# Performance work log

Hardware: AMD Instinct MI355X
Metric: run time of the kernel (lower is better)

The kernel has to match this reference:

```python
import jax, jax.numpy as jnp
import numpy as np


def setup_inputs() -> dict:
    key = jax.random.key(0)
    k1, k2, k3 = jax.random.split(key, 3)
    I, H, W, C, N = 8, 240, 320, 128, 100000
    img_feats = jax.random.normal(k1, (I, H, W, C), dtype=jnp.float32)
    pcd_feats = jax.random.normal(k2, (N, C), dtype=jnp.float32)
    # pixel coords in [0, 360): values >= H (or >= W) are masked out, mimicking
    # points that project outside the image (compute_masks)
    pcd_pixels = jax.random.randint(k3, (I, N, 2), 0, 360, dtype=jnp.int32)
    return {"img_feats": img_feats, "pcd_feats": pcd_feats, "pcd_pixels": pcd_pixels}


def reference(img_feats, pcd_feats, pcd_pixels):
    # img_feats: [I, H, W, C], pcd_feats: [N, C], pcd_pixels: [I, N, 2] (h, w)
    I, H, W, C = img_feats.shape
    N = pcd_feats.shape[0]
    h = pcd_pixels[..., 0]
    w = pcd_pixels[..., 1]
    # compute_masks: in-bounds check
    mask = (h >= 0) & (h < H) & (w >= 0) & (w < W)            # [I, N] bool
    m = mask.astype(img_feats.dtype)                          # [I, N]
    hc = jnp.clip(h, 0, H - 1)
    wc = jnp.clip(w, 0, W - 1)
    flat_hw = hc * W + wc                                     # [I, N]

    # ---- collect_img_feats: gather image feats at pixels, mean over images per point
    gathered = jnp.take_along_axis(
        img_feats.reshape(I, H * W, C), flat_hw[..., None], axis=1
    )                                                         # [I, N, C]
    pcd_counts = m.sum(axis=0)                                # [N]
    pcd_from_img = (gathered * m[..., None]).sum(axis=0) / jnp.clip(
        pcd_counts, 1e-10
    )[:, None]                                                # [N, C]

    # ---- collect_pcd_feats: scatter point feats into image grid, mean per pixel
    flat_idx = (jnp.arange(I, dtype=flat_hw.dtype)[:, None] * (H * W) + flat_hw).reshape(-1)  # [I*N]
    src = (pcd_feats[None, :, :] * m[..., None]).reshape(-1, C)                               # [I*N, C]
    img_sum = jnp.zeros((I * H * W, C), img_feats.dtype).at[flat_idx].add(src)
    img_cnt = jnp.zeros((I * H * W,), img_feats.dtype).at[flat_idx].add(m.reshape(-1))
    img_from_pcd = (img_sum / jnp.clip(img_cnt, 1e-10)[:, None]).reshape(I, H, W, C)

    return pcd_from_img, img_from_pcd
```

## Files before the change

### kernel.cpp

```cpp
#include <hip/hip_runtime.h>

#define IMGS 8
#define HH 240
#define WW 320
#define CC 128
#define HW (HH * WW)
#define ELEMS (IMGS * HW)

#define CAP 16

typedef float f4 __attribute__((ext_vector_type(4)));

__global__ __launch_bounds__(256) void zero_counts_kernel(uint4* __restrict__ p)
{
    int t = blockIdx.x * 256 + threadIdx.x;
    if (t < ELEMS / 4) p[t] = make_uint4(0u, 0u, 0u, 0u);
}

__global__ __launch_bounds__(256) void count_fill_kernel(
    const int* __restrict__ pix,
    unsigned*  __restrict__ counts,
    unsigned*  __restrict__ list,
    int N)
{
    int n = blockIdx.x * 256 + threadIdx.x;
    int i = blockIdx.y;
    if (n >= N) return;
    int2 hw = *reinterpret_cast<const int2*>(pix + ((size_t)i * N + n) * 2);
    int h = hw.x, w = hw.y;
    if (h >= 0 && h < HH && w >= 0 && w < WW) {
        int p = i * HW + h * WW + w;
        unsigned slot = atomicAdd(&counts[p], 1u);
        if (slot < CAP) list[(size_t)p * CAP + slot] = (unsigned)n;
    }
}

#define GB 12500
#define TOTAL 89600

__global__ __launch_bounds__(256) void mega_kernel(
    const float*    __restrict__ img,
    const int*      __restrict__ pix,
    const float*    __restrict__ pcd,
    const unsigned* __restrict__ counts,
    const unsigned* __restrict__ list,
    float*          __restrict__ out_pcd,
    float*          __restrict__ out_img,
    int N)
{
    int bid = blockIdx.x;
    if (bid % 7 == 0) {
        int gb = bid / 7;
        if (gb >= GB) return;
        int tid   = gb * 256 + threadIdx.x;
        int point = tid >> 5;
        int lane  = tid & 31;

        int2 hw[IMGS];
#pragma unroll
        for (int i = 0; i < IMGS; ++i)
            hw[i] = *reinterpret_cast<const int2*>(pix + ((size_t)i * N + point) * 2);

        f4    v[IMGS];
        float m[IMGS];
#pragma unroll
        for (int i = 0; i < IMGS; ++i) {
            int h = hw[i].x, w = hw[i].y;
            bool ok = (h >= 0) & (h < HH) & (w >= 0) & (w < WW);
            int hc = min(max(h, 0), HH - 1);
            int wc = min(max(w, 0), WW - 1);
            v[i] = reinterpret_cast<const f4*>(
                       img + ((size_t)i * HW + (size_t)hc * WW + wc) * CC)[lane];
            m[i] = ok ? 1.f : 0.f;
        }

        f4 acc = {0.f, 0.f, 0.f, 0.f};
        float cnt = 0.f;
#pragma unroll
        for (int i = 0; i < IMGS; ++i) {
            acc += v[i] * m[i];
            cnt += m[i];
        }
        float inv = 1.f / fmaxf(cnt, 1e-10f);
        acc *= inv;
        __builtin_nontemporal_store(
            acc, reinterpret_cast<f4*>(out_pcd + (size_t)point * CC) + lane);
    } else {
        int ob   = bid - bid / 7 - 1;
        int tid  = ob * 256 + threadIdx.x;
        int p    = tid >> 5;
        int lane = tid & 31;

        unsigned kc = counts[p];
        unsigned k  = kc < CAP ? kc : CAP;
        const uint4* lp4 = reinterpret_cast<const uint4*>(list + (size_t)p * CAP);

        f4 acc = {0.f, 0.f, 0.f, 0.f};
        for (unsigned base = 0; base < k; base += 4) {
            uint4 L = lp4[base >> 2];
            unsigned id[4] = {L.x, L.y, L.z, L.w};
            f4 v[4];
#pragma unroll
            for (int t = 0; t < 4; ++t) {
                unsigned idx = (base + t < k) ? id[t] : id[0];
                v[t] = reinterpret_cast<const f4*>(pcd + (size_t)idx * CC)[lane];
            }
#pragma unroll
            for (int t = 0; t < 4; ++t)
                acc += v[t] * ((base + t < k) ? 1.f : 0.f);
        }
        float inv = 1.f / fmaxf((float)kc, 1e-10f);
        acc *= inv;
        __builtin_nontemporal_store(
            acc, reinterpret_cast<f4*>(out_img + (size_t)p * CC) + lane);
    }
}

__global__ __launch_bounds__(256) void gather_kernel(
    const float* __restrict__ img, const int* __restrict__ pix,
    float* __restrict__ out, int N)
{
    int tid   = blockIdx.x * blockDim.x + threadIdx.x;
    int point = tid >> 5;
    int lane  = tid & 31;
    if (point >= N) return;
    f4 acc = {0.f, 0.f, 0.f, 0.f};
    float cnt = 0.f;
#pragma unroll
    for (int i = 0; i < IMGS; ++i) {
        int2 hw = *reinterpret_cast<const int2*>(pix + ((size_t)i * N + point) * 2);
        int h = hw.x, w = hw.y;
        if (h >= 0 && h < HH && w >= 0 && w < WW) {
            acc += reinterpret_cast<const f4*>(
                img + ((size_t)i * HW + (size_t)h * WW + w) * CC)[lane];
            cnt += 1.f;
        }
    }
    float inv = 1.f / fmaxf(cnt, 1e-10f);
    acc *= inv;
    reinterpret_cast<f4*>(out + (size_t)point * CC)[lane] = acc;
}

__global__ __launch_bounds__(256) void scatter_kernel(
    const float* __restrict__ pcd, const int* __restrict__ pix,
    float* __restrict__ img_sum, float* __restrict__ cnt, int N)
{
    int n = blockIdx.x * 2 + (threadIdx.x >> 7);
    int c = threadIdx.x & 127;
    int i = blockIdx.y;
    if (n >= N) return;
    int2 hw = *reinterpret_cast<const int2*>(pix + ((size_t)i * N + n) * 2);
    int h = hw.x, w = hw.y;
    if (h >= 0 && h < HH && w >= 0 && w < WW) {
        size_t p = (size_t)i * HW + (size_t)h * WW + w;
        atomicAdd(&img_sum[p * CC + c], pcd[(size_t)n * CC + c]);
        if (c == 0) atomicAdd(&cnt[p], 1.f);
    }
}

__global__ __launch_bounds__(256) void normalize_kernel(
    float* __restrict__ img_sum, const float* __restrict__ cnt)
{
    int tid  = blockIdx.x * blockDim.x + threadIdx.x;
    int pixI = tid >> 5;
    int lane = tid & 31;
    if (pixI >= ELEMS) return;
    float inv = 1.f / fmaxf(cnt[pixI], 1e-10f);
    f4* p = reinterpret_cast<f4*>(img_sum + (size_t)pixI * CC) + lane;
    f4 v = *p;
    v *= inv;
    *p = v;
}

extern "C" void kernel_launch(void* const* d_in, const int* in_sizes, int n_in,
                              void* d_out, int out_size, void* d_ws, size_t ws_size,
                              hipStream_t stream)
{
    const float* img_feats  = (const float*)d_in[0];
    const float* pcd_feats  = (const float*)d_in[1];
    const int*   pcd_pixels = (const int*)d_in[2];

    const int N = in_sizes[1] / CC;

    float* out_pcd = (float*)d_out;
    float* out_img = out_pcd + (size_t)N * CC;

    size_t need = (size_t)ELEMS * 4
                + (size_t)ELEMS * CAP * 4;

    if (ws_size >= need) {
        unsigned* counts = (unsigned*)d_ws;
        unsigned* list   = counts + ELEMS;

        zero_counts_kernel<<<(ELEMS / 4 + 255) / 256, 256, 0, stream>>>((uint4*)counts);

        dim3 pgrid((N + 255) / 256, IMGS, 1);
        count_fill_kernel<<<pgrid, 256, 0, stream>>>(pcd_pixels, counts, list, N);

        mega_kernel<<<TOTAL, 256, 0, stream>>>(
            img_feats, pcd_pixels, pcd_feats, counts, list, out_pcd, out_img, N);
    } else {
        {
            int blocks = (N * 32 + 255) / 256;
            gather_kernel<<<blocks, 256, 0, stream>>>(img_feats, pcd_pixels, out_pcd, N);
        }
        float* cnt = (float*)d_ws;
        hipMemsetAsync(out_img, 0, (size_t)ELEMS * CC * sizeof(float), stream);
        hipMemsetAsync(cnt,     0, (size_t)ELEMS * sizeof(float), stream);
        dim3 sgrid((N + 1) / 2, IMGS, 1);
        scatter_kernel<<<sgrid, 256, 0, stream>>>(pcd_feats, pcd_pixels, out_img, cnt, N);
        long long t = (long long)ELEMS * 32;
        int blocks  = (int)((t + 255) / 256);
        normalize_kernel<<<blocks, 256, 0, stream>>>(out_img, cnt);
    }
}
```

Baseline: 192.3 us.

## Precompute packed per-point pixel offsets in prep kernel and peel first list chunk

The count/fill kernel now handles all images per point in one thread and writes a packed offset array, holding the clamped flat offset with the mask in the top bit, 8 per point. The gather path reads these 32 bytes instead of recomputing offsets from strided pixel coordinates, and a sched barrier groups its loads ahead of the sums. The scatter-gather path loads the first list chunk before checking the count and peels the first iteration. This trades an extra workspace write and read for less index math and fewer scattered coordinate loads, but the prep kernel now serialises 8 atomics per thread.

```diff
diff --git a/kernel.cpp b/kernel.cpp
--- a/kernel.cpp
+++ b/kernel.cpp
@@ -17,31 +17,43 @@
     if (t < ELEMS / 4) p[t] = make_uint4(0u, 0u, 0u, 0u);
 }
 
-__global__ __launch_bounds__(256) void count_fill_kernel(
+__global__ __launch_bounds__(256) void prep_count_fill_kernel(
     const int* __restrict__ pix,
     unsigned*  __restrict__ counts,
     unsigned*  __restrict__ list,
+    unsigned*  __restrict__ poff,
     int N)
 {
     int n = blockIdx.x * 256 + threadIdx.x;
-    int i = blockIdx.y;
     if (n >= N) return;
-    int2 hw = *reinterpret_cast<const int2*>(pix + ((size_t)i * N + n) * 2);
-    int h = hw.x, w = hw.y;
-    if (h >= 0 && h < HH && w >= 0 && w < WW) {
-        int p = i * HW + h * WW + w;
-        unsigned slot = atomicAdd(&counts[p], 1u);
-        if (slot < CAP) list[(size_t)p * CAP + slot] = (unsigned)n;
-    }
+
+    unsigned po[IMGS];
+#pragma unroll
+    for (int i = 0; i < IMGS; ++i) {
+        int2 hw = *reinterpret_cast<const int2*>(pix + ((size_t)i * N + n) * 2);
+        int h = hw.x, w = hw.y;
+        bool ok = (h >= 0) & (h < HH) & (w >= 0) & (w < WW);
+        int hc = min(max(h, 0), HH - 1);
+        int wc = min(max(w, 0), WW - 1);
+        unsigned off = (unsigned)(i * HW + hc * WW + wc);
+        po[i] = off | (ok ? 0x80000000u : 0u);
+        if (ok) {
+            unsigned slot = atomicAdd(&counts[off], 1u);
+            if (slot < CAP) list[(size_t)off * CAP + slot] = (unsigned)n;
+        }
+    }
+    uint4* dst = reinterpret_cast<uint4*>(poff + (size_t)n * IMGS);
+    dst[0] = make_uint4(po[0], po[1], po[2], po[3]);
+    dst[1] = make_uint4(po[4], po[5], po[6], po[7]);
 }
 
 #define GB 12500
 #define TOTAL 89600
 
 __global__ __launch_bounds__(256) void mega_kernel(
-    const float*    __restrict__ img,
-    const int*      __restrict__ pix,
-    const float*    __restrict__ pcd,
+    const f4*       __restrict__ img4,
+    const unsigned* __restrict__ poff,
+    const f4*       __restrict__ pcd4,
     const unsigned* __restrict__ counts,
     const unsigned* __restrict__ list,
     float*          __restrict__ out_pcd,
@@ -55,24 +67,21 @@
         int tid   = gb * 256 + threadIdx.x;
         int point = tid >> 5;
         int lane  = tid & 31;
-
-        int2 hw[IMGS];
-#pragma unroll
-        for (int i = 0; i < IMGS; ++i)
-            hw[i] = *reinterpret_cast<const int2*>(pix + ((size_t)i * N + point) * 2);
+        if (point >= N) return;
+
+        const uint4* pp = reinterpret_cast<const uint4*>(poff + (size_t)point * IMGS);
+        uint4 pa = pp[0], pb = pp[1];
+        unsigned po[IMGS] = {pa.x, pa.y, pa.z, pa.w, pb.x, pb.y, pb.z, pb.w};
 
         f4    v[IMGS];
         float m[IMGS];
 #pragma unroll
         for (int i = 0; i < IMGS; ++i) {
-            int h = hw[i].x, w = hw[i].y;
-            bool ok = (h >= 0) & (h < HH) & (w >= 0) & (w < WW);
-            int hc = min(max(h, 0), HH - 1);
-            int wc = min(max(w, 0), WW - 1);
-            v[i] = reinterpret_cast<const f4*>(
-                       img + ((size_t)i * HW + (size_t)hc * WW + wc) * CC)[lane];
-            m[i] = ok ? 1.f : 0.f;
-        }
+            unsigned off = po[i] & 0x7fffffffu;
+            v[i] = img4[(size_t)off * 32u + (unsigned)lane];
+            m[i] = (po[i] & 0x80000000u) ? 1.f : 0.f;
+        }
+        __builtin_amdgcn_sched_barrier(0);
 
         f4 acc = {0.f, 0.f, 0.f, 0.f};
         float cnt = 0.f;
@@ -92,22 +101,35 @@
         int lane = tid & 31;
 
         unsigned kc = counts[p];
-        unsigned k  = kc < CAP ? kc : CAP;
-        const uint4* lp4 = reinterpret_cast<const uint4*>(list + (size_t)p * CAP);
-
+        uint4 L = reinterpret_cast<const uint4*>(list + (size_t)p * CAP)[0];
+
+        unsigned k = kc < CAP ? kc : CAP;
         f4 acc = {0.f, 0.f, 0.f, 0.f};
-        for (unsigned base = 0; base < k; base += 4) {
-            uint4 L = lp4[base >> 2];
+        if (k) {
             unsigned id[4] = {L.x, L.y, L.z, L.w};
             f4 v[4];
 #pragma unroll
             for (int t = 0; t < 4; ++t) {
-                unsigned idx = (base + t < k) ? id[t] : id[0];
-                v[t] = reinterpret_cast<const f4*>(pcd + (size_t)idx * CC)[lane];
+                unsigned idx = ((unsigned)t < k) ? id[t] : id[0];
+                v[t] = pcd4[(size_t)idx * 32u + (unsigned)lane];
             }
 #pragma unroll
             for (int t = 0; t < 4; ++t)
-                acc += v[t] * ((base + t < k) ? 1.f : 0.f);
+                acc += v[t] * (((unsigned)t < k) ? 1.f : 0.f);
+
+            for (unsigned base = 4; base < k; base += 4) {
+                uint4 L2 = reinterpret_cast<const uint4*>(list + (size_t)p * CAP)[base >> 2];
+                unsigned id2[4] = {L2.x, L2.y, L2.z, L2.w};
+                f4 v2[4];
+#pragma unroll
+                for (int t = 0; t < 4; ++t) {
+                    unsigned idx = (base + t < k) ? id2[t] : id2[0];
+                    v2[t] = pcd4[(size_t)idx * 32u + (unsigned)lane];
+                }
+#pragma unroll
+                for (int t = 0; t < 4; ++t)
+                    acc += v2[t] * ((base + t < k) ? 1.f : 0.f);
+            }
         }
         float inv = 1.f / fmaxf((float)kc, 1e-10f);
         acc *= inv;
@@ -186,19 +208,22 @@
     float* out_img = out_pcd + (size_t)N * CC;
 
     size_t need = (size_t)ELEMS * 4
-                + (size_t)ELEMS * CAP * 4;
+                + (size_t)ELEMS * CAP * 4
+                + (size_t)N * IMGS * 4;
 
     if (ws_size >= need) {
         unsigned* counts = (unsigned*)d_ws;
         unsigned* list   = counts + ELEMS;
+        unsigned* poff   = list + (size_t)ELEMS * CAP;
 
         zero_counts_kernel<<<(ELEMS / 4 + 255) / 256, 256, 0, stream>>>((uint4*)counts);
 
-        dim3 pgrid((N + 255) / 256, IMGS, 1);
-        count_fill_kernel<<<pgrid, 256, 0, stream>>>(pcd_pixels, counts, list, N);
+        prep_count_fill_kernel<<<(N + 255) / 256, 256, 0, stream>>>(
+            pcd_pixels, counts, list, poff, N);
 
         mega_kernel<<<TOTAL, 256, 0, stream>>>(
-            img_feats, pcd_pixels, pcd_feats, counts, list, out_pcd, out_img, N);
+            (const f4*)img_feats, poff, (const f4*)pcd_feats,
+            counts, list, out_pcd, out_img, N);
     } else {
         {
             int blocks = (N * 32 + 255) / 256;
```

After: 189.9 us. About the same (-1.2%).
